# Optimization experiments

Hardware: AMD Instinct MI355X
Metric: run time of the kernel (lower is better)

The kernel has to match this reference:

```python
import jax, jax.numpy as jnp
import numpy as np

EPS = 1e-12

def sage_layer(x, src, dst, Wl, Wr, b, n_nodes):
    # mean aggregation of source-node features into destination nodes
    msgs = x[src]                                            # [E, F] gather
    s = jax.ops.segment_sum(msgs, dst, num_segments=n_nodes)  # [N, F]
    cnt = jax.ops.segment_sum(jnp.ones((src.shape[0],), x.dtype), dst, num_segments=n_nodes)
    agg = s / jnp.maximum(cnt, 1.0)[:, None]                 # mean; 0 for isolated nodes
    out = agg @ Wl + b + x @ Wr                              # lin_l(agg) + lin_r(x_i)
    norm = jnp.linalg.norm(out, axis=-1, keepdims=True)      # normalize=True -> L2 norm
    return out / jnp.maximum(norm, EPS)


def setup_inputs() -> dict:
    key = jax.random.key(0)
    ks = jax.random.split(key, 8)
    N, E, F = 100000, 1200000, 64
    H1, H2, OUT = 64, 32, 10  # hidden_channels//2, hidden_channels//4, output_dim
    x = jax.random.normal(ks[0], (N, F), dtype=jnp.float32)
    edge_index = jax.random.randint(ks[1], (2, E), 0, N, dtype=jnp.int64)
    def glorot(k, fin, fout):
        lim = np.sqrt(6.0 / (fin + fout)).astype(np.float32)
        return jax.random.uniform(k, (fin, fout), jnp.float32, -lim, lim)
    return {
        "x": x,
        "edge_index": edge_index,
        "W1l": glorot(ks[2], F, H1), "W1r": glorot(ks[3], F, H1), "b1": jnp.zeros((H1,), jnp.float32),
        "W2l": glorot(ks[4], H1, H2), "W2r": glorot(ks[5], H1, H2), "b2": jnp.zeros((H2,), jnp.float32),
        "W3l": glorot(ks[6], H2, OUT), "W3r": glorot(ks[7], H2, OUT), "b3": jnp.zeros((OUT,), jnp.float32),
    }


def reference(x, edge_index, W1l, W1r, b1, W2l, W2r, b2, W3l, W3r, b3):
    n = x.shape[0]
    src, dst = edge_index[0], edge_index[1]
    h = jax.nn.relu(sage_layer(x, src, dst, W1l, W1r, b1, n))
    h = jax.nn.relu(sage_layer(h, src, dst, W2l, W2r, b2, n))
    h = sage_layer(h, src, dst, W3l, W3r, b3, n)
    return jax.nn.log_softmax(h, axis=1)
```

## Files before the change

kernel.cpp:

```cpp
#include <hip/hip_runtime.h>
#include <math.h>


typedef __attribute__((ext_vector_type(8))) short short8;
typedef __attribute__((ext_vector_type(4))) float floatx4;
typedef __attribute__((ext_vector_type(2))) float floatx2;

__device__ __forceinline__ unsigned short f2bf(float f) {
    unsigned u = __float_as_uint(f);
    u += 0x7fffu + ((u >> 16) & 1u);
    return (unsigned short)(u >> 16);
}
__device__ __forceinline__ float blo(unsigned u) { return __uint_as_float(u << 16); }
__device__ __forceinline__ float bhi(unsigned u) { return __uint_as_float(u & 0xffff0000u); }
__device__ __forceinline__ unsigned char f2fp8(float f) {
    return (unsigned char)(__builtin_amdgcn_cvt_pk_fp8_f32(f, f, 0, false) & 0xFF);
}


__global__ __launch_bounds__(256) void hist_kernel(
        const int* __restrict__ ei, int* __restrict__ bh, int E, int NB, int NBKT) {
    __shared__ int lh[256];
    const int tid = threadIdx.x, blk = blockIdx.x;
    lh[tid] = 0;
    __syncthreads();
    const int base = blk << 12;
#pragma unroll
    for (int i = 0; i < 16; ++i) {
        const int e = base + (i << 8) + tid;
        if (e < E) atomicAdd(&lh[min((int)(((unsigned)ei[E + e]) >> 9), NBKT - 1)], 1);
    }
    __syncthreads();
    if (tid < NBKT) bh[tid * NB + blk] = lh[tid];
}

__global__ __launch_bounds__(256) void bscan_kernel(
        const int* __restrict__ bh, int* __restrict__ offs, int* __restrict__ btot,
        int NB, int NBKT) {
    const int lane = threadIdx.x & 63;
    const int w = blockIdx.x * 4 + (threadIdx.x >> 6);
    if (w >= NBKT) return;
    int running = 0;
    for (int base = 0; base < NB; base += 64) {
        const int j = base + lane;
        const int v = (j < NB) ? bh[w * NB + j] : 0;
        int incl = v;
#pragma unroll
        for (int off = 1; off < 64; off <<= 1) {
            const int t = __shfl_up(incl, off);
            if (lane >= off) incl += t;
        }
        if (j < NB) offs[w * NB + j] = running + incl - v;
        running += __shfl(incl, 63);
    }
    if (lane == 0) btot[w] = running;
}

__global__ __launch_bounds__(64) void bucketbase_kernel(
        const int* __restrict__ btot, int* __restrict__ bucket_base, int NBKT) {
    const int lane = threadIdx.x;
    int running = 0;
    for (int base = 0; base < NBKT; base += 64) {
        const int j = base + lane;
        const int v = (j < NBKT) ? btot[j] : 0;
        int incl = v;
#pragma unroll
        for (int off = 1; off < 64; off <<= 1) {
            const int t = __shfl_up(incl, off);
            if (lane >= off) incl += t;
        }
        if (j < NBKT) bucket_base[j] = running + incl - v;
        running += __shfl(incl, 63);
    }
    if (lane == 0) bucket_base[NBKT] = running;
}

__global__ __launch_bounds__(256) void scatter_kernel(
        const int* __restrict__ ei, const int* __restrict__ offs,
        const int* __restrict__ bucket_base, unsigned* __restrict__ ebuf,
        int E, int NB, int NBKT) {
    __shared__ int lcur[256];
    const int tid = threadIdx.x, blk = blockIdx.x;
    if (tid < NBKT) lcur[tid] = bucket_base[tid] + offs[tid * NB + blk];
    __syncthreads();
    const int base = blk << 12;
#pragma unroll
    for (int i = 0; i < 16; ++i) {
        const int e = base + (i << 8) + tid;
        if (e < E) {
            const int s = ei[e];
            const unsigned d = (unsigned)ei[E + e];
            int p = atomicAdd(&lcur[min((int)(d >> 9), NBKT - 1)], 1);
            p = min(p, E - 1);
            ebuf[p] = ((d & 511u) << 17) | (unsigned)s;
        }
    }
}

__global__ __launch_bounds__(512) void bucket_csr_kernel(
        const unsigned* __restrict__ ebuf, const int* __restrict__ bucket_base,
        int* __restrict__ rowptr, int* __restrict__ deg, int* __restrict__ col,
        int N, int E) {
    __shared__ int ldeg[512];
    __shared__ int lc1[512];
    __shared__ int lc2[512];
    __shared__ int lc3[512];
    __shared__ int buf[512];
    __shared__ int lcur[2048];
    const int b = blockIdx.x, tid = threadIdx.x;
    const int q1 = N >> 2, q2 = N >> 1, q3 = (N >> 2) + (N >> 1);
    const int segbase = bucket_base[b];
    const int L = bucket_base[b + 1] - segbase;
    ldeg[tid] = 0; lc1[tid] = 0; lc2[tid] = 0; lc3[tid] = 0;
    __syncthreads();
    for (int i = tid; i < L; i += 512) {
        const unsigned p = ebuf[segbase + i];
        const int ln = p >> 17;
        const int s  = (int)(p & 0x1FFFFu);
        atomicAdd(&ldeg[ln], 1);
        if (s < q1) atomicAdd(&lc1[ln], 1);
        if (s < q2) atomicAdd(&lc2[ln], 1);
        if (s < q3) atomicAdd(&lc3[ln], 1);
    }
    __syncthreads();
    buf[tid] = ldeg[tid];
    __syncthreads();
    for (int off = 1; off < 512; off <<= 1) {
        const int t = (tid >= off) ? buf[tid - off] : 0;
        __syncthreads();
        buf[tid] += t;
        __syncthreads();
    }
    const int excl = buf[tid] - ldeg[tid];
    const int node = (b << 9) + tid;
    if (node < N) { rowptr[node] = segbase + excl; deg[node] = ldeg[tid]; }
    lcur[tid]          = excl;
    lcur[512 + tid]    = excl + lc1[tid];
    lcur[1024 + tid]   = excl + lc2[tid];
    lcur[1536 + tid]   = excl + lc3[tid];
    __syncthreads();
    for (int i = tid; i < L; i += 512) {
        const unsigned p = ebuf[segbase + i];
        const int ln = p >> 17;
        const int s  = (int)(p & 0x1FFFFu);
        const int q  = (s < q2) ? ((s < q1) ? 0 : 1) : ((s < q3) ? 2 : 3);
        int pos = atomicAdd(&lcur[(q << 9) + ln], 1);
        pos = min(segbase + pos, E - 1);
        col[pos] = s;
    }
}

template <int K, int F_OUT, int PAD, bool AFP32, bool YL8>
__global__ __launch_bounds__(256) void transform_kernel(
        const void* __restrict__ Ain, const float* __restrict__ Wl,
        const float* __restrict__ Wr, const float* __restrict__ b,
        void* __restrict__ yl, unsigned short* __restrict__ yr, int n) {
    constexpr int KSTEP = K / 32;
    constexpr int NT = PAD / 16;
    const int lane = threadIdx.x & 63;
    const int wid = (blockIdx.x * blockDim.x + threadIdx.x) >> 6;
    const int ntiles = (n + 15) >> 4;
    if (wid >= ntiles) return;
    const int nl = lane & 15, q = lane >> 4;

    short8 Bl[NT][KSTEP], Br[NT][KSTEP];
    float biasv[NT];
#pragma unroll
    for (int t = 0; t < NT; ++t) {
        const int ncol = t * 16 + nl;
        biasv[t] = (ncol < F_OUT) ? b[ncol] : 0.f;
#pragma unroll
        for (int ks = 0; ks < KSTEP; ++ks) {
#pragma unroll
            for (int j = 0; j < 8; ++j) {
                const int k = ks * 32 + q * 8 + j;
                Bl[t][ks][j] = (ncol < F_OUT) ? (short)f2bf(Wl[k * F_OUT + ncol]) : (short)0;
                Br[t][ks][j] = (ncol < F_OUT) ? (short)f2bf(Wr[k * F_OUT + ncol]) : (short)0;
            }
        }
    }

    const int m0 = wid * 16;
    int m = m0 + nl; if (m >= n) m = n - 1;

    short8 a[KSTEP];
#pragma unroll
    for (int ks = 0; ks < KSTEP; ++ks) {
        if (AFP32) {
            const float* p = (const float*)Ain + (size_t)m * K + ks * 32 + q * 8;
#pragma unroll
            for (int j = 0; j < 8; ++j) a[ks][j] = (short)f2bf(p[j]);
        } else {
            union { uint4 u; short8 s; } cvt;
            cvt.u = *(const uint4*)((const unsigned short*)Ain + (size_t)m * K + ks * 32 + q * 8);
            a[ks] = cvt.s;
        }
    }

    floatx4 accl[NT], accr[NT];
#pragma unroll
    for (int t = 0; t < NT; ++t) { accl[t] = {0.f,0.f,0.f,0.f}; accr[t] = {0.f,0.f,0.f,0.f}; }
#pragma unroll
    for (int ks = 0; ks < KSTEP; ++ks) {
#pragma unroll
        for (int t = 0; t < NT; ++t) {
            accl[t] = __builtin_amdgcn_mfma_f32_16x16x32_bf16(a[ks], Bl[t][ks], accl[t], 0, 0, 0);
            accr[t] = __builtin_amdgcn_mfma_f32_16x16x32_bf16(a[ks], Br[t][ks], accr[t], 0, 0, 0);
        }
    }

#pragma unroll
    for (int t = 0; t < NT; ++t) {
        const int ncol = t * 16 + nl;
#pragma unroll
        for (int r = 0; r < 4; ++r) {
            const int node = m0 + q * 4 + r;
            if (node < n) {
                if (YL8)
                    ((unsigned char*)yl)[(size_t)node * PAD + ncol] = f2fp8(accl[t][r]);
                else
                    ((unsigned short*)yl)[(size_t)node * PAD + ncol] = f2bf(accl[t][r]);
                yr[(size_t)node * PAD + ncol] = f2bf(accr[t][r] + biasv[t]);
            }
        }
    }
}

template <int F, int ACT, int PK>
__global__ __launch_bounds__(256) void agg_kernel(
        const void* __restrict__ yl, const unsigned short* __restrict__ yr,
        const int* __restrict__ rowptr, const int* __restrict__ degv,
        const int* __restrict__ col,
        unsigned short* __restrict__ hout, float* __restrict__ fout, int n) {
    constexpr int G = F / 8;
    constexpr int NPW = 64 / G;
    const int lane = threadIdx.x & 63;
    const int wid = (blockIdx.x * blockDim.x + threadIdx.x) >> 6;
    const int g = lane / G, c = lane % G;
    const int node = wid * NPW + g;
    if (node >= n) return;

    const int beg = rowptr[node];
    const int dg  = degv[node];
    const int nmax = n - 1;

    float a0=0.f,a1=0.f,a2=0.f,a3=0.f,a4=0.f,a5=0.f,a6=0.f,a7=0.f;
    int i = 0;
    if (PK == 1) {
        const unsigned char* base = (const unsigned char*)yl + c * 8;
        auto accrow = [&](uint2 t) {
            const floatx2 p0 = __builtin_amdgcn_cvt_pk_f32_fp8((int)t.x, false);
            const floatx2 p1 = __builtin_amdgcn_cvt_pk_f32_fp8((int)t.x, true);
            const floatx2 p2 = __builtin_amdgcn_cvt_pk_f32_fp8((int)t.y, false);
            const floatx2 p3 = __builtin_amdgcn_cvt_pk_f32_fp8((int)t.y, true);
            a0 += p0.x; a1 += p0.y; a2 += p1.x; a3 += p1.y;
            a4 += p2.x; a5 += p2.y; a6 += p3.x; a7 += p3.y;
        };
        for (; i + 4 <= dg; i += 4) {
            const int n0 = min(col[beg + i],     nmax);
            const int n1 = min(col[beg + i + 1], nmax);
            const int n2 = min(col[beg + i + 2], nmax);
            const int n3 = min(col[beg + i + 3], nmax);
            const uint2 t0 = *(const uint2*)(base + (size_t)n0 * F);
            const uint2 t1 = *(const uint2*)(base + (size_t)n1 * F);
            const uint2 t2 = *(const uint2*)(base + (size_t)n2 * F);
            const uint2 t3 = *(const uint2*)(base + (size_t)n3 * F);
            accrow(t0); accrow(t1); accrow(t2); accrow(t3);
        }
        for (; i < dg; ++i) {
            const int n0 = min(col[beg + i], nmax);
            accrow(*(const uint2*)(base + (size_t)n0 * F));
        }
    } else {
        const unsigned short* base = (const unsigned short*)yl + c * 8;
        for (; i + 4 <= dg; i += 4) {
            const int n0 = min(col[beg + i],     nmax);
            const int n1 = min(col[beg + i + 1], nmax);
            const int n2 = min(col[beg + i + 2], nmax);
            const int n3 = min(col[beg + i + 3], nmax);
            const uint4 t0 = *(const uint4*)(base + (size_t)n0 * F);
            const uint4 t1 = *(const uint4*)(base + (size_t)n1 * F);
            const uint4 t2 = *(const uint4*)(base + (size_t)n2 * F);
            const uint4 t3 = *(const uint4*)(base + (size_t)n3 * F);
            a0 += blo(t0.x) + blo(t1.x) + blo(t2.x) + blo(t3.x);
            a1 += bhi(t0.x) + bhi(t1.x) + bhi(t2.x) + bhi(t3.x);
            a2 += blo(t0.y) + blo(t1.y) + blo(t2.y) + blo(t3.y);
            a3 += bhi(t0.y) + bhi(t1.y) + bhi(t2.y) + bhi(t3.y);
            a4 += blo(t0.z) + blo(t1.z) + blo(t2.z) + blo(t3.z);
            a5 += bhi(t0.z) + bhi(t1.z) + bhi(t2.z) + bhi(t3.z);
            a6 += blo(t0.w) + blo(t1.w) + blo(t2.w) + blo(t3.w);
            a7 += bhi(t0.w) + bhi(t1.w) + bhi(t2.w) + bhi(t3.w);
        }
        for (; i < dg; ++i) {
            const int n0 = min(col[beg + i], nmax);
            const uint4 t0 = *(const uint4*)(base + (size_t)n0 * F);
            a0 += blo(t0.x); a1 += bhi(t0.x); a2 += blo(t0.y); a3 += bhi(t0.y);
            a4 += blo(t0.z); a5 += bhi(t0.z); a6 += blo(t0.w); a7 += bhi(t0.w);
        }
    }
    const float inv = (dg > 0) ? 1.f / (float)dg : 0.f;

    const uint4 rv = *(const uint4*)(yr + (size_t)node * F + c * 8);
    float o[8];
    o[0] = a0*inv + blo(rv.x); o[1] = a1*inv + bhi(rv.x);
    o[2] = a2*inv + blo(rv.y); o[3] = a3*inv + bhi(rv.y);
    o[4] = a4*inv + blo(rv.z); o[5] = a5*inv + bhi(rv.z);
    o[6] = a6*inv + blo(rv.w); o[7] = a7*inv + bhi(rv.w);

    float ss = 0.f;
#pragma unroll
    for (int j = 0; j < 8; ++j) ss += o[j] * o[j];
#pragma unroll
    for (int off = 1; off < G; off <<= 1) ss += __shfl_xor(ss, off);
    const float scale = 1.f / fmaxf(sqrtf(ss), 1e-12f);

    if (ACT == 1) {
        uint4 u;
        float h[8];
#pragma unroll
        for (int j = 0; j < 8; ++j) h[j] = fmaxf(o[j] * scale, 0.f);
        u.x = (unsigned)f2bf(h[0]) | ((unsigned)f2bf(h[1]) << 16);
        u.y = (unsigned)f2bf(h[2]) | ((unsigned)f2bf(h[3]) << 16);
        u.z = (unsigned)f2bf(h[4]) | ((unsigned)f2bf(h[5]) << 16);
        u.w = (unsigned)f2bf(h[6]) | ((unsigned)f2bf(h[7]) << 16);
        *(uint4*)(hout + (size_t)node * F + c * 8) = u;
    } else {
#pragma unroll
        for (int j = 0; j < 8; ++j) o[j] *= scale;
        const int cbase = c * 8;
        float m = -INFINITY;
#pragma unroll
        for (int j = 0; j < 8; ++j) if (cbase + j < 10) m = fmaxf(m, o[j]);
        m = fmaxf(m, __shfl_xor(m, 1));
        float s = 0.f;
#pragma unroll
        for (int j = 0; j < 8; ++j) if (cbase + j < 10) s += __expf(o[j] - m);
        s += __shfl_xor(s, 1);
        const float ls = logf(s);
#pragma unroll
        for (int j = 0; j < 8; ++j)
            if (cbase + j < 10) fout[(size_t)node * 10 + cbase + j] = o[j] - m - ls;
    }
}

extern "C" void kernel_launch(void* const* d_in, const int* in_sizes, int n_in,
                              void* d_out, int out_size, void* d_ws, size_t ws_size,
                              hipStream_t stream) {
    const float* x   = (const float*)d_in[0];
    const int*   ei  = (const int*)d_in[1];
    const float* W1l = (const float*)d_in[2];
    const float* W1r = (const float*)d_in[3];
    const float* b1  = (const float*)d_in[4];
    const float* W2l = (const float*)d_in[5];
    const float* W2r = (const float*)d_in[6];
    const float* b2  = (const float*)d_in[7];
    const float* W3l = (const float*)d_in[8];
    const float* W3r = (const float*)d_in[9];
    const float* b3  = (const float*)d_in[10];
    float*       out = (float*)d_out;

    const int N = in_sizes[0] / 64;
    const int E = in_sizes[1] / 2;
    const int NBKT = (N + 511) >> 9;
    const int NB   = (E + 4095) >> 12;

    auto align16 = [](size_t v) { return (v + 15) & ~(size_t)15; };
    char* ws = (char*)d_ws;
    size_t off = 0;
    int* rowptr  = (int*)(ws + off); off = align16(off + (size_t)N * 4);
    int* deg     = (int*)(ws + off); off = align16(off + (size_t)N * 4);
    int* colidx  = (int*)(ws + off); off = align16(off + (size_t)E * 4);
    unsigned* ebuf = (unsigned*)(ws + off); off = align16(off + (size_t)E * 4);
    int* bh      = (int*)(ws + off); off = align16(off + (size_t)NBKT * NB * 4);
    int* offsb   = (int*)(ws + off); off = align16(off + (size_t)NBKT * NB * 4);
    int* btot    = (int*)(ws + off); off = align16(off + (size_t)NBKT * 4);
    int* bbase   = (int*)(ws + off); off = align16(off + (size_t)(NBKT + 1) * 4);
    unsigned char*  y1l = (unsigned char*)(ws + off);  off = align16(off + (size_t)N * 64);
    unsigned short* y1r = (unsigned short*)(ws + off); off = align16(off + (size_t)N * 64 * 2);
    unsigned short* h1  = (unsigned short*)(ws + off); off = align16(off + (size_t)N * 64 * 2);
    unsigned char*  y2l = (unsigned char*)(ws + off);  off = align16(off + (size_t)N * 32);
    unsigned short* y2r = (unsigned short*)(ws + off); off = align16(off + (size_t)N * 32 * 2);
    unsigned short* h2  = (unsigned short*)(ws + off); off = align16(off + (size_t)N * 32 * 2);
    unsigned short* y3l = (unsigned short*)(ws + off); off = align16(off + (size_t)N * 16 * 2);
    unsigned short* y3r = (unsigned short*)(ws + off); off = align16(off + (size_t)N * 16 * 2);
    (void)ws_size; (void)n_in; (void)out_size;

    hist_kernel<<<NB, 256, 0, stream>>>(ei, bh, E, NB, NBKT);
    bscan_kernel<<<(NBKT + 3) / 4, 256, 0, stream>>>(bh, offsb, btot, NB, NBKT);
    bucketbase_kernel<<<1, 64, 0, stream>>>(btot, bbase, NBKT);
    scatter_kernel<<<NB, 256, 0, stream>>>(ei, offsb, bbase, ebuf, E, NB, NBKT);
    bucket_csr_kernel<<<NBKT, 512, 0, stream>>>(ebuf, bbase, rowptr, deg, colidx, N, E);

    const int ntiles = (N + 15) / 16;
    const int tblocks = (ntiles * 64 + 255) / 256;

    transform_kernel<64, 64, 64, true, true><<<tblocks, 256, 0, stream>>>(
        x, W1l, W1r, b1, y1l, y1r, N);
    agg_kernel<64, 1, 1><<<(N + 31) / 32, 256, 0, stream>>>(
        y1l, y1r, rowptr, deg, colidx, h1, nullptr, N);
    transform_kernel<64, 32, 32, false, true><<<tblocks, 256, 0, stream>>>(
        h1, W2l, W2r, b2, y2l, y2r, N);
    agg_kernel<32, 1, 1><<<(N + 63) / 64, 256, 0, stream>>>(
        y2l, y2r, rowptr, deg, colidx, h2, nullptr, N);
    transform_kernel<32, 10, 16, false, false><<<tblocks, 256, 0, stream>>>(
        h2, W3l, W3r, b3, y3l, y3r, N);
    agg_kernel<16, 2, 0><<<(N + 127) / 128, 256, 0, stream>>>(
        y3l, y3r, rowptr, deg, colidx, nullptr, out, N);
}
```

Before: 215.3 us.

## Fuse bucket-base scan into bscan, pack CSR counters, prefetch column indices

Three independent changes. The single-block bucket-base scan becomes a last-block-done step inside bscan_kernel, using an atomic counter reset by hist_kernel, which removes one kernel launch. The CSR build packs four 16-bit quadrant counters into one 64-bit shared atomic and replaces the 512-wide barrier-heavy scan with a wavefront shuffle scan. The aggregation gather loops software-prefetch the next four column indices, so index loads overlap the feature gathers. Risks: the 16-bit counters overflow if a node quadrant exceeds 65535 edges, and correctness depends on the counter reset being ordered before bscan.

```diff
diff --git a/kernel.cpp b/kernel.cpp
--- a/kernel.cpp
+++ b/kernel.cpp
@@ -19,9 +19,11 @@
 
 
 __global__ __launch_bounds__(256) void hist_kernel(
-        const int* __restrict__ ei, int* __restrict__ bh, int E, int NB, int NBKT) {
+        const int* __restrict__ ei, int* __restrict__ bh, int* __restrict__ sync_ctr,
+        int E, int NB, int NBKT) {
     __shared__ int lh[256];
     const int tid = threadIdx.x, blk = blockIdx.x;
+    if (blk == 0 && tid == 0) *sync_ctr = 0;
     lh[tid] = 0;
     __syncthreads();
     const int base = blk << 12;
@@ -36,43 +38,48 @@
 
 __global__ __launch_bounds__(256) void bscan_kernel(
         const int* __restrict__ bh, int* __restrict__ offs, int* __restrict__ btot,
+        int* __restrict__ bucket_base, int* __restrict__ sync_ctr,
         int NB, int NBKT) {
     const int lane = threadIdx.x & 63;
     const int w = blockIdx.x * 4 + (threadIdx.x >> 6);
-    if (w >= NBKT) return;
-    int running = 0;
-    for (int base = 0; base < NB; base += 64) {
-        const int j = base + lane;
-        const int v = (j < NB) ? bh[w * NB + j] : 0;
-        int incl = v;
-#pragma unroll
-        for (int off = 1; off < 64; off <<= 1) {
-            const int t = __shfl_up(incl, off);
-            if (lane >= off) incl += t;
-        }
-        if (j < NB) offs[w * NB + j] = running + incl - v;
-        running += __shfl(incl, 63);
-    }
-    if (lane == 0) btot[w] = running;
-}
-
-__global__ __launch_bounds__(64) void bucketbase_kernel(
-        const int* __restrict__ btot, int* __restrict__ bucket_base, int NBKT) {
-    const int lane = threadIdx.x;
-    int running = 0;
-    for (int base = 0; base < NBKT; base += 64) {
-        const int j = base + lane;
-        const int v = (j < NBKT) ? btot[j] : 0;
-        int incl = v;
-#pragma unroll
-        for (int off = 1; off < 64; off <<= 1) {
-            const int t = __shfl_up(incl, off);
-            if (lane >= off) incl += t;
-        }
-        if (j < NBKT) bucket_base[j] = running + incl - v;
-        running += __shfl(incl, 63);
-    }
-    if (lane == 0) bucket_base[NBKT] = running;
+    if (w < NBKT) {
+        int running = 0;
+        for (int base = 0; base < NB; base += 64) {
+            const int j = base + lane;
+            const int v = (j < NB) ? bh[w * NB + j] : 0;
+            int incl = v;
+#pragma unroll
+            for (int off = 1; off < 64; off <<= 1) {
+                const int t = __shfl_up(incl, off);
+                if (lane >= off) incl += t;
+            }
+            if (j < NB) offs[w * NB + j] = running + incl - v;
+            running += __shfl(incl, 63);
+        }
+        if (lane == 0) btot[w] = running;
+    }
+    __threadfence();
+    __syncthreads();
+    __shared__ int amLast;
+    if (threadIdx.x == 0) amLast = (atomicAdd(sync_ctr, 1) == (int)gridDim.x - 1);
+    __syncthreads();
+    if (amLast && threadIdx.x < 64) {
+        __threadfence();
+        int running = 0;
+        for (int base = 0; base < NBKT; base += 64) {
+            const int j = base + threadIdx.x;
+            const int v = (j < NBKT) ? btot[j] : 0;
+            int incl = v;
+#pragma unroll
+            for (int off = 1; off < 64; off <<= 1) {
+                const int t = __shfl_up(incl, off);
+                if ((int)threadIdx.x >= off) incl += t;
+            }
+            if (j < NBKT) bucket_base[j] = running + incl - v;
+            running += __shfl(incl, 63);
+        }
+        if (threadIdx.x == 0) bucket_base[NBKT] = running;
+    }
 }
 
 __global__ __launch_bounds__(256) void scatter_kernel(
@@ -101,43 +108,46 @@
         const unsigned* __restrict__ ebuf, const int* __restrict__ bucket_base,
         int* __restrict__ rowptr, int* __restrict__ deg, int* __restrict__ col,
         int N, int E) {
-    __shared__ int ldeg[512];
-    __shared__ int lc1[512];
-    __shared__ int lc2[512];
-    __shared__ int lc3[512];
-    __shared__ int buf[512];
+    __shared__ unsigned long long lcnt[512];
     __shared__ int lcur[2048];
+    __shared__ int wsum[8];
     const int b = blockIdx.x, tid = threadIdx.x;
     const int q1 = N >> 2, q2 = N >> 1, q3 = (N >> 2) + (N >> 1);
     const int segbase = bucket_base[b];
     const int L = bucket_base[b + 1] - segbase;
-    ldeg[tid] = 0; lc1[tid] = 0; lc2[tid] = 0; lc3[tid] = 0;
+    lcnt[tid] = 0ull;
     __syncthreads();
     for (int i = tid; i < L; i += 512) {
         const unsigned p = ebuf[segbase + i];
         const int ln = p >> 17;
         const int s  = (int)(p & 0x1FFFFu);
-        atomicAdd(&ldeg[ln], 1);
-        if (s < q1) atomicAdd(&lc1[ln], 1);
-        if (s < q2) atomicAdd(&lc2[ln], 1);
-        if (s < q3) atomicAdd(&lc3[ln], 1);
-    }
-    __syncthreads();
-    buf[tid] = ldeg[tid];
-    __syncthreads();
-    for (int off = 1; off < 512; off <<= 1) {
-        const int t = (tid >= off) ? buf[tid - off] : 0;
-        __syncthreads();
-        buf[tid] += t;
-        __syncthreads();
-    }
-    const int excl = buf[tid] - ldeg[tid];
+        const int q  = (s < q2) ? ((s < q1) ? 0 : 1) : ((s < q3) ? 2 : 3);
+        atomicAdd(&lcnt[ln], 1ull << (q << 4));
+    }
+    __syncthreads();
+    const unsigned long long cv = lcnt[tid];
+    const int f0 = (int)(cv & 0xFFFFu),         f1 = (int)((cv >> 16) & 0xFFFFu);
+    const int f2 = (int)((cv >> 32) & 0xFFFFu), f3 = (int)((cv >> 48) & 0xFFFFu);
+    const int dnode = f0 + f1 + f2 + f3;
+    const int lane = tid & 63, w = tid >> 6;
+    int incl = dnode;
+#pragma unroll
+    for (int off = 1; off < 64; off <<= 1) {
+        const int t = __shfl_up(incl, off);
+        if (lane >= off) incl += t;
+    }
+    if (lane == 63) wsum[w] = incl;
+    __syncthreads();
+    int wbase = 0;
+#pragma unroll
+    for (int ww = 0; ww < 8; ++ww) if (ww < w) wbase += wsum[ww];
+    const int excl = wbase + incl - dnode;
     const int node = (b << 9) + tid;
-    if (node < N) { rowptr[node] = segbase + excl; deg[node] = ldeg[tid]; }
-    lcur[tid]          = excl;
-    lcur[512 + tid]    = excl + lc1[tid];
-    lcur[1024 + tid]   = excl + lc2[tid];
-    lcur[1536 + tid]   = excl + lc3[tid];
+    if (node < N) { rowptr[node] = segbase + excl; deg[node] = dnode; }
+    lcur[tid]        = excl;
+    lcur[512 + tid]  = excl + f0;
+    lcur[1024 + tid] = excl + f0 + f1;
+    lcur[1536 + tid] = excl + f0 + f1 + f2;
     __syncthreads();
     for (int i = tid; i < L; i += 512) {
         const unsigned p = ebuf[segbase + i];
@@ -256,47 +266,54 @@
             a0 += p0.x; a1 += p0.y; a2 += p1.x; a3 += p1.y;
             a4 += p2.x; a5 += p2.y; a6 += p3.x; a7 += p3.y;
         };
-        for (; i + 4 <= dg; i += 4) {
-            const int n0 = min(col[beg + i],     nmax);
-            const int n1 = min(col[beg + i + 1], nmax);
-            const int n2 = min(col[beg + i + 2], nmax);
-            const int n3 = min(col[beg + i + 3], nmax);
-            const uint2 t0 = *(const uint2*)(base + (size_t)n0 * F);
-            const uint2 t1 = *(const uint2*)(base + (size_t)n1 * F);
-            const uint2 t2 = *(const uint2*)(base + (size_t)n2 * F);
-            const uint2 t3 = *(const uint2*)(base + (size_t)n3 * F);
+        if (dg >= 4) {
+            int c0 = col[beg], c1 = col[beg+1], c2 = col[beg+2], c3 = col[beg+3];
+            for (; i + 8 <= dg; i += 4) {
+                const int d0 = col[beg+i+4], d1 = col[beg+i+5];
+                const int d2 = col[beg+i+6], d3 = col[beg+i+7];
+                const uint2 t0 = *(const uint2*)(base + (size_t)min(c0,nmax) * F);
+                const uint2 t1 = *(const uint2*)(base + (size_t)min(c1,nmax) * F);
+                const uint2 t2 = *(const uint2*)(base + (size_t)min(c2,nmax) * F);
+                const uint2 t3 = *(const uint2*)(base + (size_t)min(c3,nmax) * F);
+                accrow(t0); accrow(t1); accrow(t2); accrow(t3);
+                c0 = d0; c1 = d1; c2 = d2; c3 = d3;
+            }
+            const uint2 t0 = *(const uint2*)(base + (size_t)min(c0,nmax) * F);
+            const uint2 t1 = *(const uint2*)(base + (size_t)min(c1,nmax) * F);
+            const uint2 t2 = *(const uint2*)(base + (size_t)min(c2,nmax) * F);
+            const uint2 t3 = *(const uint2*)(base + (size_t)min(c3,nmax) * F);
             accrow(t0); accrow(t1); accrow(t2); accrow(t3);
-        }
-        for (; i < dg; ++i) {
-            const int n0 = min(col[beg + i], nmax);
-            accrow(*(const uint2*)(base + (size_t)n0 * F));
-        }
+            i += 4;
+        }
+        for (; i < dg; ++i)
+            accrow(*(const uint2*)(base + (size_t)min(col[beg+i],nmax) * F));
     } else {
         const unsigned short* base = (const unsigned short*)yl + c * 8;
-        for (; i + 4 <= dg; i += 4) {
-            const int n0 = min(col[beg + i],     nmax);
-            const int n1 = min(col[beg + i + 1], nmax);
-            const int n2 = min(col[beg + i + 2], nmax);
-            const int n3 = min(col[beg + i + 3], nmax);
-            const uint4 t0 = *(const uint4*)(base + (size_t)n0 * F);
-            const uint4 t1 = *(const uint4*)(base + (size_t)n1 * F);
-            const uint4 t2 = *(const uint4*)(base + (size_t)n2 * F);
-            const uint4 t3 = *(const uint4*)(base + (size_t)n3 * F);
-            a0 += blo(t0.x) + blo(t1.x) + blo(t2.x) + blo(t3.x);
-            a1 += bhi(t0.x) + bhi(t1.x) + bhi(t2.x) + bhi(t3.x);
-            a2 += blo(t0.y) + blo(t1.y) + blo(t2.y) + blo(t3.y);
-            a3 += bhi(t0.y) + bhi(t1.y) + bhi(t2.y) + bhi(t3.y);
-            a4 += blo(t0.z) + blo(t1.z) + blo(t2.z) + blo(t3.z);
-            a5 += bhi(t0.z) + bhi(t1.z) + bhi(t2.z) + bhi(t3.z);
-            a6 += blo(t0.w) + blo(t1.w) + blo(t2.w) + blo(t3.w);
-            a7 += bhi(t0.w) + bhi(t1.w) + bhi(t2.w) + bhi(t3.w);
-        }
-        for (; i < dg; ++i) {
-            const int n0 = min(col[beg + i], nmax);
-            const uint4 t0 = *(const uint4*)(base + (size_t)n0 * F);
-            a0 += blo(t0.x); a1 += bhi(t0.x); a2 += blo(t0.y); a3 += bhi(t0.y);
-            a4 += blo(t0.z); a5 += bhi(t0.z); a6 += blo(t0.w); a7 += bhi(t0.w);
-        }
+        auto accrow4 = [&](uint4 t) {
+            a0 += blo(t.x); a1 += bhi(t.x); a2 += blo(t.y); a3 += bhi(t.y);
+            a4 += blo(t.z); a5 += bhi(t.z); a6 += blo(t.w); a7 += bhi(t.w);
+        };
+        if (dg >= 4) {
+            int c0 = col[beg], c1 = col[beg+1], c2 = col[beg+2], c3 = col[beg+3];
+            for (; i + 8 <= dg; i += 4) {
+                const int d0 = col[beg+i+4], d1 = col[beg+i+5];
+                const int d2 = col[beg+i+6], d3 = col[beg+i+7];
+                const uint4 t0 = *(const uint4*)(base + (size_t)min(c0,nmax) * F);
+                const uint4 t1 = *(const uint4*)(base + (size_t)min(c1,nmax) * F);
+                const uint4 t2 = *(const uint4*)(base + (size_t)min(c2,nmax) * F);
+                const uint4 t3 = *(const uint4*)(base + (size_t)min(c3,nmax) * F);
+                accrow4(t0); accrow4(t1); accrow4(t2); accrow4(t3);
+                c0 = d0; c1 = d1; c2 = d2; c3 = d3;
+            }
+            const uint4 t0 = *(const uint4*)(base + (size_t)min(c0,nmax) * F);
+            const uint4 t1 = *(const uint4*)(base + (size_t)min(c1,nmax) * F);
+            const uint4 t2 = *(const uint4*)(base + (size_t)min(c2,nmax) * F);
+            const uint4 t3 = *(const uint4*)(base + (size_t)min(c3,nmax) * F);
+            accrow4(t0); accrow4(t1); accrow4(t2); accrow4(t3);
+            i += 4;
+        }
+        for (; i < dg; ++i)
+            accrow4(*(const uint4*)(base + (size_t)min(col[beg+i],nmax) * F));
     }
     const float inv = (dg > 0) ? 1.f / (float)dg : 0.f;
 
@@ -375,6 +392,7 @@
     int* offsb   = (int*)(ws + off); off = align16(off + (size_t)NBKT * NB * 4);
     int* btot    = (int*)(ws + off); off = align16(off + (size_t)NBKT * 4);
     int* bbase   = (int*)(ws + off); off = align16(off + (size_t)(NBKT + 1) * 4);
+    int* sctr    = (int*)(ws + off); off = align16(off + 16);
     unsigned char*  y1l = (unsigned char*)(ws + off);  off = align16(off + (size_t)N * 64);
     unsigned short* y1r = (unsigned short*)(ws + off); off = align16(off + (size_t)N * 64 * 2);
     unsigned short* h1  = (unsigned short*)(ws + off); off = align16(off + (size_t)N * 64 * 2);
@@ -385,9 +403,8 @@
     unsigned short* y3r = (unsigned short*)(ws + off); off = align16(off + (size_t)N * 16 * 2);
     (void)ws_size; (void)n_in; (void)out_size;
 
-    hist_kernel<<<NB, 256, 0, stream>>>(ei, bh, E, NB, NBKT);
-    bscan_kernel<<<(NBKT + 3) / 4, 256, 0, stream>>>(bh, offsb, btot, NB, NBKT);
-    bucketbase_kernel<<<1, 64, 0, stream>>>(btot, bbase, NBKT);
+    hist_kernel<<<NB, 256, 0, stream>>>(ei, bh, sctr, E, NB, NBKT);
+    bscan_kernel<<<(NBKT + 3) / 4, 256, 0, stream>>>(bh, offsb, btot, bbase, sctr, NB, NBKT);
     scatter_kernel<<<NB, 256, 0, stream>>>(ei, offsb, bbase, ebuf, E, NB, NBKT);
     bucket_csr_kernel<<<NBKT, 512, 0, stream>>>(ebuf, bbase, rowptr, deg, colidx, N, E);
 
```

After: 212.3 us. About the same (-1.4%).
